# Optimization experiments

Hardware: AMD Instinct MI355X
Metric: run time of the kernel (lower is better)

The kernel has to match this reference:

```python
import jax, jax.numpy as jnp
import numpy as np

G_DCN = 32   # DCNv2 conv groups
KSZ = 3      # kernel size
P = KSZ * KSZ  # 9 sampling points
G_POST = 256  # post 1x1 conv groups
C_OUT = 2048


def _dcnv2(x, w_off, b_off, w_dcn, b_dcn):
    """Modulated deformable conv v2 (stride 1, pad 1, deformable_groups=1)."""
    B, C, H, W = x.shape
    # offset/mask branch: 3x3 conv -> 27 channels = (dy[9], dx[9], mask[9])
    off = jax.lax.conv_general_dilated(
        x, w_off, (1, 1), ((1, 1), (1, 1)),
        dimension_numbers=('NCHW', 'OIHW', 'NCHW')) + b_off[None, :, None, None]
    dy, dx = off[:, :P], off[:, P:2 * P]
    m = jax.nn.sigmoid(off[:, 2 * P:])            # [B,P,H,W] modulation mask
    ky = (jnp.arange(P) // KSZ - 1).astype(x.dtype)  # kernel row offsets -1,0,1
    kx = (jnp.arange(P) % KSZ - 1).astype(x.dtype)
    hh = jnp.arange(H, dtype=x.dtype)[None, None, :, None]
    ww = jnp.arange(W, dtype=x.dtype)[None, None, None, :]
    sy = hh + ky[None, :, None, None] + dy        # [B,P,H,W] sample rows
    sx = ww + kx[None, :, None, None] + dx        # [B,P,H,W] sample cols
    y0f = jnp.floor(sy); x0f = jnp.floor(sx)
    wy = sy - y0f; wx = sx - x0f
    y0 = y0f.astype(jnp.int32); x0 = x0f.astype(jnp.int32)
    flat = x.reshape(B, C, H * W)

    def corner(yi, xi):
        ok = ((yi >= 0) & (yi < H) & (xi >= 0) & (xi < W)).astype(x.dtype)
        idx = (jnp.clip(yi, 0, H - 1) * W + jnp.clip(xi, 0, W - 1)).reshape(B, -1)
        v = jax.vmap(lambda f, i: f[:, i])(flat, idx).reshape(B, C, P, H, W)
        return v * ok[:, None]

    val = (corner(y0, x0) * ((1 - wy) * (1 - wx))[:, None]
           + corner(y0, x0 + 1) * ((1 - wy) * wx)[:, None]
           + corner(y0 + 1, x0) * (wy * (1 - wx))[:, None]
           + corner(y0 + 1, x0 + 1) * (wy * wx)[:, None])
    val = val * m[:, None]                        # [B,C,P,H,W]
    in_pg = C // G_DCN
    out_pg = w_dcn.shape[0] // G_DCN
    xs = val.reshape(B, G_DCN, in_pg, P, H, W)
    ws = w_dcn.reshape(G_DCN, out_pg, in_pg, P)
    out = jnp.einsum('bgiphw,goip->bgohw', xs, ws).reshape(B, -1, H, W)
    return out + b_dcn[None, :, None, None]


def setup_inputs() -> dict:
    key = jax.random.key(0)
    ks = jax.random.split(key, 8)
    lo_res = jax.random.normal(ks[0], (2, 2048, 32, 32), dtype=jnp.float32)
    hi_res = jax.random.normal(ks[1], (2, 1024, 64, 64), dtype=jnp.float32)
    # offset conv weights kept small so sampled locations stay near the grid
    w_off = jax.random.normal(ks[2], (27, 1024, 3, 3), dtype=jnp.float32) * 0.01
    b_off = jnp.zeros((27,), dtype=jnp.float32)
    w_dcn = jax.random.normal(ks[3], (1024, 32, 3, 3), dtype=jnp.float32) * (1.0 / np.sqrt(32 * 9))
    b_dcn = jax.random.normal(ks[4], (1024,), dtype=jnp.float32) * 0.01
    w_post = jax.random.normal(ks[5], (2048, 12), dtype=jnp.float32) * (1.0 / np.sqrt(12))
    b_post = jax.random.normal(ks[6], (2048,), dtype=jnp.float32) * 0.01
    return {"lo_res": lo_res, "hi_res": hi_res, "w_off": w_off, "b_off": b_off,
            "w_dcn": w_dcn, "b_dcn": b_dcn, "w_post": w_post, "b_post": b_post}


def reference(lo_res, hi_res, w_off, b_off, w_dcn, b_dcn, w_post, b_post):
    B, Clo, h, w = lo_res.shape
    # policy=0: bilinear x2 upsample (align_corners=False == half-pixel, jax default)
    lo_up = jax.image.resize(lo_res, (B, Clo, 2 * h, 2 * w), method='bilinear')
    hi_al = _dcnv2(hi_res, w_off, b_off, w_dcn, b_dcn)
    x = jnp.concatenate([lo_up, hi_al], axis=1)   # [B,3072,H,W]
    H, W = x.shape[2], x.shape[3]
    in_pg = x.shape[1] // G_POST                  # 12
    out_pg = C_OUT // G_POST                      # 8
    xs = x.reshape(B, G_POST, in_pg, H, W)
    ws = w_post.reshape(G_POST, out_pg, in_pg)
    out = jnp.einsum('bgihw,goi->bgohw', xs, ws).reshape(B, C_OUT, H, W)
    return out + b_post[None, :, None, None]
```

## Files before the change

### kernel.cpp

```cpp
#include <hip/hip_runtime.h>
#include <hip/hip_fp16.h>
#include <cstdint>

static constexpr size_t OFF_XT   = 0;
static constexpr size_t OFF_HIAL = 16777216;
static constexpr size_t OFF_PART = OFF_HIAL;
static constexpr size_t OFF_MU   = OFF_HIAL + 33554432;
static constexpr size_t OFF_WA   = OFF_MU  + 2ull*9*4096*16;
static constexpr size_t OFF_WB   = OFF_WA  + 36864ull*16;

using f16x8 = __attribute__((ext_vector_type(8))) _Float16;
typedef __attribute__((ext_vector_type(4))) float f32x4;
typedef __attribute__((ext_vector_type(2))) float f32x2;

__device__ __forceinline__ uint16_t f2h(float f) { return __half_as_ushort(__float2half(f)); }
__device__ __forceinline__ __half2 u2h(uint32_t u) { union { uint32_t u; __half2 h; } x; x.u = u; return x.h; }
__device__ __forceinline__ uint32_t h2u(__half2 h) { union { uint32_t u; __half2 h; } x; x.h = h; return x.u; }

__device__ __forceinline__ f16x8 blend4h(uint4 A, uint4 B, uint4 C, uint4 D,
                                         __half2 wab, __half2 wcd) {
    __half2 h00 = __half2half2(__low2half(wab));
    __half2 h01 = __half2half2(__high2half(wab));
    __half2 h10 = __half2half2(__low2half(wcd));
    __half2 h11 = __half2half2(__high2half(wcd));
    const uint32_t* a = (const uint32_t*)&A;
    const uint32_t* b = (const uint32_t*)&B;
    const uint32_t* c = (const uint32_t*)&C;
    const uint32_t* d = (const uint32_t*)&D;
    union { uint32_t u[4]; f16x8 v; } r;
#pragma unroll
    for (int e = 0; e < 4; ++e) {
        __half2 acc = __hmul2(h00, u2h(a[e]));
        acc = __hfma2(h01, u2h(b[e]), acc);
        acc = __hfma2(h10, u2h(c[e]), acc);
        acc = __hfma2(h11, u2h(d[e]), acc);
        r.u[e] = h2u(acc);
    }
    return r.v;
}

__global__ void k_prep(const float* __restrict__ w_off, const float* __restrict__ w_dcn,
                       uint4* __restrict__ waT, uint32_t* __restrict__ wb) {
    int idx = blockIdx.x * 256 + threadIdx.x;
    if (idx < 36864) {
        int kg = idx & 3, col = (idx >> 2) & 15, mt = (idx >> 6) & 1;
        int ks = (idx >> 7) & 3, kc = (idx >> 9) & 7, p = idx >> 12;
        int oc = mt * 16 + col;
        int chb = kc * 128 + ks * 32 + kg * 8;
        union { uint32_t u[4]; uint4 v; } r;
#pragma unroll
        for (int e = 0; e < 4; ++e) {
            uint32_t lo = 0, hi = 0;
            if (oc < 27) {
                lo = f2h(w_off[(size_t)oc * 9216 + (size_t)(chb + 2 * e) * 9 + p]);
                hi = f2h(w_off[(size_t)oc * 9216 + (size_t)(chb + 2 * e + 1) * 9 + p]);
            }
            r.u[e] = lo | (hi << 16);
        }
        waT[idx] = r.v;
    } else {
        int j = idx - 36864;
        if (j >= 32 * 9 * 32 * 16) return;
        int g = j / (9 * 32 * 16), r = j % (9 * 32 * 16);
        int p = r / (32 * 16), r2 = r % (32 * 16), o = r2 / 16, ip = r2 % 16;
        uint32_t lo = f2h(w_dcn[((size_t)(g * 32 + o) * 32 + 2 * ip) * 9 + p]);
        uint32_t hi = f2h(w_dcn[((size_t)(g * 32 + o) * 32 + 2 * ip + 1) * 9 + p]);
        wb[j] = lo | (hi << 16);
    }
}

__global__ void k_transpose(const float* __restrict__ x, uint32_t* __restrict__ xt) {
    __shared__ float tile[64][65];
    int cblk = blockIdx.x * 64, y = blockIdx.y, b = blockIdx.z, t = threadIdx.x;
    const float* src = x + ((size_t)(b * 1024 + cblk)) * 4096 + y * 64;
#pragma unroll
    for (int k = 0; k < 16; ++k) {
        int lin = t + k * 256;
        int cl = lin >> 6, xx = lin & 63;
        tile[cl][xx] = src[(size_t)cl * 4096 + xx];
    }
    __syncthreads();
    int kc = cblk >> 7, half = (cblk & 64) >> 1;
    uint32_t* dst = xt + ((size_t)(b * 8 + kc) * 4096 + (size_t)y * 64) * 64 + half;
#pragma unroll
    for (int k = 0; k < 8; ++k) {
        int lin = t + k * 256;
        int xx = lin >> 5, cp = lin & 31;
        uint32_t lo = f2h(tile[2 * cp][xx]);
        uint32_t hi = f2h(tile[2 * cp + 1][xx]);
        dst[(size_t)xx * 64 + cp] = lo | (hi << 16);
    }
}

__global__ __launch_bounds__(256, 4) void k_offconv_mfma(const uint32_t* __restrict__ xt,
                                                         const uint4* __restrict__ waT,
                                                         __half* __restrict__ part) {
    __shared__ uint4 sb[1632];
    int bx = blockIdx.x;
    int y = bx >> 1, xh = bx & 1;
    int kc = blockIdx.y, b = blockIdx.z;
    int t = threadIdx.x, wave = t >> 6, lane = t & 63;
    int pxg = wave >> 1, mt = wave & 1;
    int col = lane & 15, kg = lane >> 4;

    {
        const uint32_t* srcb = xt + ((size_t)(b * 8 + kc) * 4096) * 64;
#pragma unroll
        for (int i = 0; i < 7; ++i) {
            int idx = i * 256 + t;
            if (idx < 1632) {
                int s = idx >> 4, q = idx & 15;
                int rr = s >= 68 ? 2 : (s >= 34 ? 1 : 0);
                int pxl = s - rr * 34;
                int gy = y - 1 + rr, gx = xh * 32 - 1 + pxl;
                uint4 val = uint4{0, 0, 0, 0};
                if (gy >= 0 && gy < 64 && gx >= 0 && gx < 64)
                    val = *(const uint4*)(srcb + ((size_t)(gy * 64 + gx)) * 64 + q * 4);
                sb[s * 16 + (q ^ (s & 15))] = val;
            }
        }
    }
    __syncthreads();

    f32x4 acc[9];
#pragma unroll
    for (int p = 0; p < 9; ++p) acc[p] = f32x4{0.f, 0.f, 0.f, 0.f};

#pragma unroll
    for (int p = 0; p < 9; ++p) {
        int ky = p / 3 - 1, kx = p % 3 - 1;
        int pxl = pxg * 16 + col + kx + 1;
        int s = (ky + 1) * 34 + pxl;
#pragma unroll
        for (int ks = 0; ks < 4; ++ks) {
            f16x8 bfr = *(const f16x8*)&sb[s * 16 + ((ks * 4 + kg) ^ (s & 15))];
            int gidx = ((((p * 8 + kc) * 4 + ks) * 2 + mt) * 16 + col) * 4 + kg;
            f16x8 afr = *(const f16x8*)&waT[gidx];
            acc[p] = __builtin_amdgcn_mfma_f32_16x16x32_f16(afr, bfr, acc[p], 0, 0, 0);
        }
    }

    int px = y * 64 + xh * 32 + pxg * 16 + col;
    int ocl = mt * 16 + kg * 4;
#pragma unroll
    for (int p = 0; p < 9; ++p) {
        __half* pc = part + ((size_t)((kc * 9 + p) * 2 + b)) * 28 * 4096 + px;
#pragma unroll
        for (int j = 0; j < 4; ++j)
            if (ocl + j < 28) pc[(size_t)(ocl + j) * 4096] = __float2half(acc[p][j]);
    }
}

__global__ void k_meta(const __half* __restrict__ part, const float* __restrict__ b_off,
                       uint4* __restrict__ mu) {
    int idx = blockIdx.x * 256 + threadIdx.x;
    if (idx >= 2 * 9 * 4096) return;
    int b = idx / (9 * 4096), r = idx % (9 * 4096), p = r / 4096, hw = r % 4096;
    int h = hw >> 6, w = hw & 63;
    float sdy = b_off[p], sdx = b_off[p + 9], sm = b_off[p + 18];
#pragma unroll 4
    for (int s = 0; s < 72; ++s) {
        const __half* pb = part + ((size_t)(s * 2 + b)) * 28 * 4096 + hw;
        sdy += __half2float(pb[(size_t)p * 4096]);
        sdx += __half2float(pb[(size_t)(p + 9) * 4096]);
        sm  += __half2float(pb[(size_t)(p + 18) * 4096]);
    }
    float m = 1.f / (1.f + expf(-sm));
    int ky = p / 3 - 1, kx = p % 3 - 1;
    float sy = (float)(h + ky) + sdy;
    float sx = (float)(w + kx) + sdx;
    float y0f = floorf(sy), x0f = floorf(sx);
    float wy = sy - y0f, wx = sx - x0f;
    int y0 = (int)fminf(fmaxf(y0f, -2.f), 64.f);
    int x0 = (int)fminf(fmaxf(x0f, -2.f), 64.f);
    bool vy0 = (y0 >= 0) && (y0 < 64), vy1 = (y0 + 1 >= 0) && (y0 + 1 < 64);
    bool vx0 = (x0 >= 0) && (x0 < 64), vx1 = (x0 + 1 >= 0) && (x0 + 1 < 64);
    float w00 = (1.f - wy) * (1.f - wx) * m * ((vy0 && vx0) ? 1.f : 0.f);
    float w01 = (1.f - wy) * wx         * m * ((vy0 && vx1) ? 1.f : 0.f);
    float w10 = wy * (1.f - wx)         * m * ((vy1 && vx0) ? 1.f : 0.f);
    float w11 = wy * wx                 * m * ((vy1 && vx1) ? 1.f : 0.f);
    int cy0 = min(max(y0, 0), 63),     cx0 = min(max(x0, 0), 63);
    int cy1 = min(max(y0 + 1, 0), 63), cx1 = min(max(x0 + 1, 0), 63);
    int blo = (h >> 3) * 8 - 6;
    blo = blo < 0 ? 0 : (blo > 44 ? 44 : blo);
    int blo64 = blo * 64;
    int s0 = cy0 * 64 + cx0 - blo64, s1 = cy0 * 64 + cx1 - blo64;
    int s2 = cy1 * 64 + cx0 - blo64, s3 = cy1 * 64 + cx1 - blo64;
    uint32_t wlo = (uint32_t)f2h(w00) | ((uint32_t)f2h(w01) << 16);
    uint32_t whi = (uint32_t)f2h(w10) | ((uint32_t)f2h(w11) << 16);
    uint32_t ilo = ((uint32_t)(uint16_t)(short)s0) | (((uint32_t)(uint16_t)(short)s1) << 16);
    uint32_t ihi = ((uint32_t)(uint16_t)(short)s2) | (((uint32_t)(uint16_t)(short)s3) << 16);
    mu[idx] = uint4{wlo, whi, ilo, ihi};
}

__global__ __launch_bounds__(512, 4) void k_dcn_lds(const uint32_t* __restrict__ xt,
                                                    const uint32_t* __restrict__ wb,
                                                    const uint4* __restrict__ mu,
                                                    const float* __restrict__ b_dcn,
                                                    float* __restrict__ hial) {
    __shared__ uint4 ldsq[5120];
    int g = blockIdx.x, band = blockIdx.y, b = blockIdx.z;
    int y0 = band * 8;
    int band_lo = y0 - 6;
    if (band_lo < 0) band_lo = 0;
    if (band_lo > 44) band_lo = 44;
    int t = threadIdx.x;

    {
        const uint32_t* src = xt + ((size_t)(b * 8 + (g >> 2)) * 4096 + (size_t)band_lo * 64) * 64 + (g & 3) * 16;
#pragma unroll
        for (int i = 0; i < 10; ++i) {
            int Q = i * 512 + t;
            int s = Q >> 2;
            int q = (Q & 3) ^ ((s >> 1) & 3);
            ldsq[Q] = *(const uint4*)(src + (size_t)s * 64 + q * 4);
        }
    }
    __syncthreads();
    const uint32_t* ldsb = (const uint32_t*)ldsq;

    int wave = t >> 6, lane = t & 63;
    int col = lane & 15, kg = lane >> 4;
    int strip = (wave & 3) * 16;
    int rbase = (wave >> 2) * 4;
    const uint32_t* xb = xt + ((size_t)(b * 8 + (g >> 2)) * 4096) * 64 + (g & 3) * 16 + kg * 4;
    const uint32_t* wg = wb + (size_t)g * 9 * 32 * 16 + col * 16 + kg * 4;
    const uint4* mub = mu + (size_t)b * 9 * 4096;
    const float* bd  = b_dcn + g * 32;
    int blo64 = band_lo * 64;

#define LDSRD(SS) (*(const uint4*)(ldsb + (SS) * 16 + ((kg ^ (((SS) >> 1) & 3)) << 2)))
#define GSLOW(SS, U)                                                               \
    {                                                                              \
        int s_ = (SS);                                                             \
        int sc_ = s_ < 0 ? 0 : (s_ > 1279 ? 1279 : s_);                            \
        U = LDSRD(sc_);                                                            \
        if ((unsigned)s_ >= 1280u)                                                 \
            U = *(const uint4*)(xb + (size_t)(s_ + blo64) * 64);                   \
    }

    for (int r = 0; r < 4; ++r) {
        int pix = (y0 + rbase + r) * 64 + strip + col;
        f32x4 acc0 = {0.f, 0.f, 0.f, 0.f};
        f32x4 acc1 = {0.f, 0.f, 0.f, 0.f};
#pragma unroll
        for (int p = 0; p < 9; ++p) {
            uint4 cm = mub[p * 4096 + pix];
            int s0 = (short)(cm.z & 0xffffu), s1 = (short)(cm.z >> 16);
            int s2 = (short)(cm.w & 0xffffu), s3 = (short)(cm.w >> 16);
            unsigned mx = (unsigned)s0;
            mx = mx > (unsigned)s1 ? mx : (unsigned)s1;
            mx = mx > (unsigned)s2 ? mx : (unsigned)s2;
            mx = mx > (unsigned)s3 ? mx : (unsigned)s3;
            uint4 u0, u1, u2, u3;
            if (__builtin_expect(mx >= 1280u, 0)) {
                GSLOW(s0, u0)
                GSLOW(s1, u1)
                GSLOW(s2, u2)
                GSLOW(s3, u3)
            } else {
                u0 = LDSRD(s0);
                u1 = LDSRD(s1);
                u2 = LDSRD(s2);
                u3 = LDSRD(s3);
            }
            f16x8 bfr = blend4h(u0, u1, u2, u3, u2h(cm.x), u2h(cm.y));
            const uint32_t* ap = wg + (size_t)p * 512;
            f16x8 af0 = *(const f16x8*)ap;
            f16x8 af1 = *(const f16x8*)(ap + 256);
            acc0 = __builtin_amdgcn_mfma_f32_16x16x32_f16(af0, bfr, acc0, 0, 0, 0);
            acc1 = __builtin_amdgcn_mfma_f32_16x16x32_f16(af1, bfr, acc1, 0, 0, 0);
        }
        float* pc = hial + ((size_t)b * 1024 + g * 32) * 4096 + pix;
#pragma unroll
        for (int j = 0; j < 4; ++j) {
            pc[(size_t)(kg * 4 + j) * 4096]      = acc0[j] + bd[kg * 4 + j];
            pc[(size_t)(16 + kg * 4 + j) * 4096] = acc1[j] + bd[16 + kg * 4 + j];
        }
    }
#undef LDSRD
#undef GSLOW
}

__global__ __launch_bounds__(256, 4) void k_post5(const float* __restrict__ lo,
                                                  const float* __restrict__ hial,
                                                  const float* __restrict__ wp,
                                                  const float* __restrict__ bp,
                                                  float* __restrict__ out) {
    int gq = blockIdx.x, kq = blockIdx.y, b = blockIdx.z;
    int t = threadIdx.x;
    int g = __builtin_amdgcn_readfirstlane(gq * 4 + (t >> 6));
    int lane = t & 63, k = kq * 4 + (lane >> 4), w4 = lane & 15;
    int rm = k > 0 ? k - 1 : 0, rp = k < 31 ? k + 1 : 31;
    int lc = 2 * w4 - 1; lc = lc < 0 ? 0 : (lc > 28 ? 28 : lc);
    bool is0 = (w4 == 0), is15 = (w4 == 15);

    f32x4 acc0[8], acc1[8];
#pragma unroll
    for (int o = 0; o < 8; ++o) {
        float bv = bp[g * 8 + o];
        acc0[o] = f32x4{bv, bv, bv, bv};
        acc1[o] = acc0[o];
    }
    const float* wrow = wp + (size_t)g * 96;
    int cbase = g * 12;

#define UPROW(LB, R, H)                                                            \
    {                                                                              \
        f32x4 q = *(const f32x4*)((LB) + (R) * 32 + lc);                           \
        float e0 = is15 ? q.y : q.x;                                               \
        float p0 = is0 ? q.x : (is15 ? q.z : q.y);                                 \
        float p1 = is0 ? q.y : (is15 ? q.w : q.z);                                 \
        float e3 = is0 ? q.z : q.w;                                                \
        H = f32x4{0.25f * e0 + 0.75f * p0, 0.75f * p0 + 0.25f * p1,                \
                  0.25f * p0 + 0.75f * p1, 0.75f * p1 + 0.25f * e3};               \
    }
#define LOCH(I)                                                                    \
    {                                                                              \
        const float* lb = lo + ((size_t)(b * 2048 + cbase + (I))) * 1024;          \
        f32x4 hm, hk, hp;                                                          \
        UPROW(lb, rm, hm) UPROW(lb, k, hk) UPROW(lb, rp, hp)                       \
        f32x4 va = 0.25f * hm + 0.75f * hk;                                        \
        f32x4 vb = 0.75f * hk + 0.25f * hp;                                        \
        _Pragma("unroll")                                                          \
        for (int o = 0; o < 8; ++o) {                                              \
            float w = wrow[o * 12 + (I)];                                          \
            acc0[o] += w * va;                                                     \
            acc1[o] += w * vb;                                                     \
        }                                                                          \
    }
#define HICH(I)                                                                    \
    {                                                                              \
        const float* hb = hial + ((size_t)(b * 1024 + cbase + (I) - 2048)) * 4096  \
                          + (size_t)(2 * k) * 64 + 4 * w4;                         \
        f32x4 va = *(const f32x4*)hb;                                              \
        f32x4 vb = *(const f32x4*)(hb + 64);                                       \
        _Pragma("unroll")                                                          \
        for (int o = 0; o < 8; ++o) {                                              \
            float w = wrow[o * 12 + (I)];                                          \
            acc0[o] += w * va;                                                     \
            acc1[o] += w * vb;                                                     \
        }                                                                          \
    }

    if (g <= 169) {
#pragma unroll 4
        for (int i = 0; i < 12; ++i) LOCH(i)
    } else if (g >= 171) {
#pragma unroll 4
        for (int i = 0; i < 12; ++i) HICH(i)
    } else {
#pragma unroll 4
        for (int i = 0; i < 8; ++i) LOCH(i)
#pragma unroll
        for (int i = 8; i < 12; ++i) HICH(i)
    }
#undef LOCH
#undef HICH
#undef UPROW

    float* ob = out + ((size_t)(b * 2048 + g * 8)) * 4096 + (size_t)(2 * k) * 64 + 4 * w4;
#pragma unroll
    for (int o = 0; o < 8; ++o) {
        __builtin_nontemporal_store(acc0[o], (f32x4*)(ob + (size_t)o * 4096));
        __builtin_nontemporal_store(acc1[o], (f32x4*)(ob + (size_t)o * 4096 + 64));
    }
}

extern "C" void kernel_launch(void* const* d_in, const int* in_sizes, int n_in,
                              void* d_out, int out_size, void* d_ws, size_t ws_size,
                              hipStream_t stream) {
    const float* lo_res = (const float*)d_in[0];
    const float* hi_res = (const float*)d_in[1];
    const float* w_off  = (const float*)d_in[2];
    const float* b_off  = (const float*)d_in[3];
    const float* w_dcn  = (const float*)d_in[4];
    const float* b_dcn  = (const float*)d_in[5];
    const float* w_post = (const float*)d_in[6];
    const float* b_post = (const float*)d_in[7];
    float* out = (float*)d_out;
    char* ws = (char*)d_ws;

    uint32_t* xt  = (uint32_t*)(ws + OFF_XT);
    float* hial   = (float*)(ws + OFF_HIAL);
    __half* part  = (__half*)(ws + OFF_PART);
    uint4* mup    = (uint4*)(ws + OFF_MU);
    uint4* waT    = (uint4*)(ws + OFF_WA);
    uint32_t* wbp = (uint32_t*)(ws + OFF_WB);

    k_prep<<<(36864 + 32 * 9 * 32 * 16 + 255) / 256, 256, 0, stream>>>(w_off, w_dcn, waT, wbp);
    k_transpose<<<dim3(16, 64, 2), 256, 0, stream>>>(hi_res, xt);
    k_offconv_mfma<<<dim3(128, 8, 2), 256, 0, stream>>>(xt, waT, part);
    k_meta<<<(2 * 9 * 4096 + 255) / 256, 256, 0, stream>>>(part, b_off, mup);
    k_dcn_lds<<<dim3(32, 8, 2), 512, 0, stream>>>(xt, wbp, mup, b_dcn, hial);
    k_post5<<<dim3(64, 8, 2), 256, 0, stream>>>(lo_res, hial, w_post, b_post, out);
}
```

Before: 113.0 us.

## Store aligned features in fp16, split offset reduction, raise offconv occupancy

Three separate changes. The DCN output buffer (hial) is now written in half precision and read back as half in the post grouped conv, which halves that intermediate's traffic at some accuracy cost. The partial-sum reduction in k_meta moves into a separate k_sum kernel, where each thread reduces one channel over 72 slices, so there is more parallelism; this adds one launch and an fp32 sums buffer. The launch-bounds occupancy hint on the offset conv is raised from 4 to 6.

```diff
diff --git a/kernel.cpp b/kernel.cpp
--- a/kernel.cpp
+++ b/kernel.cpp
@@ -8,6 +8,7 @@
 static constexpr size_t OFF_MU   = OFF_HIAL + 33554432;
 static constexpr size_t OFF_WA   = OFF_MU  + 2ull*9*4096*16;
 static constexpr size_t OFF_WB   = OFF_WA  + 36864ull*16;
+static constexpr size_t OFF_SUM  = OFF_WB  + 147456ull*4;
 
 using f16x8 = __attribute__((ext_vector_type(8))) _Float16;
 typedef __attribute__((ext_vector_type(4))) float f32x4;
@@ -92,7 +93,7 @@
     }
 }
 
-__global__ __launch_bounds__(256, 4) void k_offconv_mfma(const uint32_t* __restrict__ xt,
+__global__ __launch_bounds__(256, 6) void k_offconv_mfma(const uint32_t* __restrict__ xt,
                                                          const uint4* __restrict__ waT,
                                                          __half* __restrict__ part) {
     __shared__ uint4 sb[1632];
@@ -151,20 +152,28 @@
     }
 }
 
-__global__ void k_meta(const __half* __restrict__ part, const float* __restrict__ b_off,
-                       uint4* __restrict__ mu) {
+__global__ void k_sum(const __half* __restrict__ part, float* __restrict__ sums) {
+    int idx = blockIdx.x * 256 + threadIdx.x;
+    if (idx >= 221184) return;
+    int st = idx / 73728, r = idx % 73728;
+    int b = r / 36864, r2 = r % 36864;
+    const __half* pb = part + (size_t)b * 28 * 4096 + (size_t)st * 36864 + r2;
+    float s = 0.f;
+#pragma unroll 8
+    for (int si = 0; si < 72; ++si)
+        s += __half2float(pb[(size_t)si * 229376]);
+    sums[idx] = s;
+}
+
+__global__ void k_meta2(const float* __restrict__ sums, const float* __restrict__ b_off,
+                        uint4* __restrict__ mu) {
     int idx = blockIdx.x * 256 + threadIdx.x;
     if (idx >= 2 * 9 * 4096) return;
     int b = idx / (9 * 4096), r = idx % (9 * 4096), p = r / 4096, hw = r % 4096;
     int h = hw >> 6, w = hw & 63;
-    float sdy = b_off[p], sdx = b_off[p + 9], sm = b_off[p + 18];
-#pragma unroll 4
-    for (int s = 0; s < 72; ++s) {
-        const __half* pb = part + ((size_t)(s * 2 + b)) * 28 * 4096 + hw;
-        sdy += __half2float(pb[(size_t)p * 4096]);
-        sdx += __half2float(pb[(size_t)(p + 9) * 4096]);
-        sm  += __half2float(pb[(size_t)(p + 18) * 4096]);
-    }
+    float sdy = b_off[p]      + sums[idx];
+    float sdx = b_off[p + 9]  + sums[73728 + idx];
+    float sm  = b_off[p + 18] + sums[147456 + idx];
     float m = 1.f / (1.f + expf(-sm));
     int ky = p / 3 - 1, kx = p % 3 - 1;
     float sy = (float)(h + ky) + sdy;
@@ -197,7 +206,7 @@
                                                     const uint32_t* __restrict__ wb,
                                                     const uint4* __restrict__ mu,
                                                     const float* __restrict__ b_dcn,
-                                                    float* __restrict__ hial) {
+                                                    __half* __restrict__ hial) {
     __shared__ uint4 ldsq[5120];
     int g = blockIdx.x, band = blockIdx.y, b = blockIdx.z;
     int y0 = band * 8;
@@ -271,11 +280,11 @@
             acc0 = __builtin_amdgcn_mfma_f32_16x16x32_f16(af0, bfr, acc0, 0, 0, 0);
             acc1 = __builtin_amdgcn_mfma_f32_16x16x32_f16(af1, bfr, acc1, 0, 0, 0);
         }
-        float* pc = hial + ((size_t)b * 1024 + g * 32) * 4096 + pix;
+        __half* pc = hial + ((size_t)b * 1024 + g * 32) * 4096 + pix;
 #pragma unroll
         for (int j = 0; j < 4; ++j) {
-            pc[(size_t)(kg * 4 + j) * 4096]      = acc0[j] + bd[kg * 4 + j];
-            pc[(size_t)(16 + kg * 4 + j) * 4096] = acc1[j] + bd[16 + kg * 4 + j];
+            pc[(size_t)(kg * 4 + j) * 4096]      = __float2half(acc0[j] + bd[kg * 4 + j]);
+            pc[(size_t)(16 + kg * 4 + j) * 4096] = __float2half(acc1[j] + bd[16 + kg * 4 + j]);
         }
     }
 #undef LDSRD
@@ -283,7 +292,7 @@
 }
 
 __global__ __launch_bounds__(256, 4) void k_post5(const float* __restrict__ lo,
-                                                  const float* __restrict__ hial,
+                                                  const __half* __restrict__ hial,
                                                   const float* __restrict__ wp,
                                                   const float* __restrict__ bp,
                                                   float* __restrict__ out) {
@@ -331,10 +340,16 @@
     }
 #define HICH(I)                                                                    \
     {                                                                              \
-        const float* hb = hial + ((size_t)(b * 1024 + cbase + (I) - 2048)) * 4096  \
+        const __half* hb = hial + ((size_t)(b * 1024 + cbase + (I) - 2048)) * 4096 \
                           + (size_t)(2 * k) * 64 + 4 * w4;                         \
-        f32x4 va = *(const f32x4*)hb;                                              \
-        f32x4 vb = *(const f32x4*)(hb + 64);                                       \
+        __half2 ha0 = *(const __half2*)(hb);                                       \
+        __half2 ha1 = *(const __half2*)(hb + 2);                                   \
+        __half2 hb0 = *(const __half2*)(hb + 64);                                  \
+        __half2 hb1 = *(const __half2*)(hb + 66);                                  \
+        f32x4 va = {__half2float(ha0.x), __half2float(ha0.y),                      \
+                    __half2float(ha1.x), __half2float(ha1.y)};                     \
+        f32x4 vb = {__half2float(hb0.x), __half2float(hb0.y),                      \
+                    __half2float(hb1.x), __half2float(hb1.y)};                     \
         _Pragma("unroll")                                                          \
         for (int o = 0; o < 8; ++o) {                                              \
             float w = wrow[o * 12 + (I)];                                          \
@@ -382,16 +397,18 @@
     char* ws = (char*)d_ws;
 
     uint32_t* xt  = (uint32_t*)(ws + OFF_XT);
-    float* hial   = (float*)(ws + OFF_HIAL);
+    __half* hial  = (__half*)(ws + OFF_HIAL);
     __half* part  = (__half*)(ws + OFF_PART);
     uint4* mup    = (uint4*)(ws + OFF_MU);
     uint4* waT    = (uint4*)(ws + OFF_WA);
     uint32_t* wbp = (uint32_t*)(ws + OFF_WB);
+    float* sums   = (float*)(ws + OFF_SUM);
 
     k_prep<<<(36864 + 32 * 9 * 32 * 16 + 255) / 256, 256, 0, stream>>>(w_off, w_dcn, waT, wbp);
     k_transpose<<<dim3(16, 64, 2), 256, 0, stream>>>(hi_res, xt);
     k_offconv_mfma<<<dim3(128, 8, 2), 256, 0, stream>>>(xt, waT, part);
-    k_meta<<<(2 * 9 * 4096 + 255) / 256, 256, 0, stream>>>(part, b_off, mup);
+    k_sum<<<(221184 + 255) / 256, 256, 0, stream>>>(part, sums);
+    k_meta2<<<(2 * 9 * 4096 + 255) / 256, 256, 0, stream>>>(sums, b_off, mup);
     k_dcn_lds<<<dim3(32, 8, 2), 512, 0, stream>>>(xt, wbp, mup, b_dcn, hial);
     k_post5<<<dim3(64, 8, 2), 256, 0, stream>>>(lo_res, hial, w_post, b_post, out);
 }
```

New measurement: 106.8 us. 1.06x faster.
